# Kernel optimization log

Measured on AMD Instinct MI355X. Metric: run time of the kernel, lower is better.

## Reference

```python
import jax, jax.numpy as jnp
import numpy as np
from jax import lax

TAU = 0.1
EPS = 1e-10


def setup_inputs() -> dict:
    key = jax.random.key(0)
    ks = jax.random.split(key, 9)
    T, B, I, H, O = 512, 128, 512, 512, 512
    std = 1.0 / np.sqrt(H)
    x = jax.random.normal(ks[0], (T, B, I), dtype=jnp.float32)
    # uniform noise for per-step gumbel-softmax sampling (training mode)
    gumbel_u = jax.random.uniform(ks[1], (T, H, 2), dtype=jnp.float32,
                                  minval=1e-6, maxval=1.0 - 1e-6)
    # parameters (orthogonal init approximated by scaled normal)
    W_in = jax.random.normal(ks[2], (H, I), dtype=jnp.float32) * std
    b_in = jax.random.normal(ks[3], (H,), dtype=jnp.float32) * std
    Wrec_free = jax.nn.relu(jax.random.normal(ks[4], (H, H), dtype=jnp.float32) * std)
    rec_bias = jax.random.normal(ks[5], (H,), dtype=jnp.float32) * std
    eimask_logit = jax.random.normal(ks[6], (H, 2), dtype=jnp.float32)
    W_out = jax.random.normal(ks[7], (O, H), dtype=jnp.float32) * std
    b_out = jax.random.normal(ks[8], (O,), dtype=jnp.float32) * std
    return {"x": x, "gumbel_u": gumbel_u, "W_in": W_in, "b_in": b_in,
            "Wrec_free": Wrec_free, "rec_bias": rec_bias,
            "eimask_logit": eimask_logit, "W_out": W_out, "b_out": b_out}


def reference(x, gumbel_u, W_in, b_in, Wrec_free, rec_bias, eimask_logit, W_out, b_out):
    # x: (T, B, I); gumbel_u: (T, H, 2)
    B = x.shape[1]
    H = W_in.shape[0]
    # gumbel-softmax (soft, tau=0.1) per timestep -> ei code in [-1, 1]
    g = -jnp.log(-jnp.log(gumbel_u + EPS) + EPS)                 # (T, H, 2)
    mask = jax.nn.softmax((eimask_logit[None] + g) / TAU, axis=-1)
    ei = mask[..., 0] - mask[..., 1]                              # (T, H)
    Wrec = jax.nn.relu(Wrec_free)                                 # (H, H)
    # precompute input gate for all steps: (T, B, H)
    ig = jnp.einsum('tbi,hi->tbh', x, W_in) + b_in

    def step(h, inp):
        ig_t, ei_t = inp
        # h @ (Wrec @ diag(ei)).T == (h * ei) @ Wrec.T
        rec_in = (h * ei_t) @ Wrec.T + rec_bias
        h_new = jax.nn.softplus(ig_t + rec_in)
        return h_new, h_new

    h0 = jnp.zeros((B, H), dtype=x.dtype)
    h_last, hs = lax.scan(step, h0, (ig, ei))                     # hs: (T, B, H)
    outputs = jnp.einsum('tbh,oh->tbo', hs, W_out) + b_out        # (T, B, O)
    c_last = jnp.zeros_like(h_last)                               # c is never updated
    return outputs, h_last, c_last
```

## Files before the change

### kernel.cpp

```cpp
#include <hip/hip_runtime.h>
#include <stdint.h>


typedef __attribute__((ext_vector_type(8))) short short8;
typedef __attribute__((ext_vector_type(4))) float f32x4;
typedef __attribute__((ext_vector_type(4))) int int4x;

__device__ __forceinline__ unsigned short f2b(float f) {
  unsigned int u = __float_as_uint(f);
  u = (u + 0x7fffu + ((u >> 16) & 1u)) >> 16;
  return (unsigned short)u;
}
__device__ __forceinline__ float b2f(unsigned short s) {
  return __uint_as_float(((unsigned int)s) << 16);
}

__global__ void prep_kernel(const float* __restrict__ gu,
                            const float* __restrict__ logit,
                            const float* __restrict__ win,
                            const float* __restrict__ wout,
                            float* __restrict__ ei,
                            unsigned short* __restrict__ winb,
                            unsigned short* __restrict__ woutb,
                            float* __restrict__ c_last) {
  int i = blockIdx.x * 256 + threadIdx.x;
  int h = i & 511;
  float u0 = gu[2 * i], u1 = gu[2 * i + 1];
  float l0 = logit[2 * h], l1 = logit[2 * h + 1];
  float g0 = -logf(-logf(u0 + 1e-10f) + 1e-10f);
  float g1 = -logf(-logf(u1 + 1e-10f) + 1e-10f);
  float dz = ((l0 + g0) - (l1 + g1)) * 10.0f;
  ei[i] = tanhf(0.5f * dz);
  winb[i]  = f2b(win[i]);
  woutb[i] = f2b(wout[i]);
  if (i < 65536) c_last[i] = 0.0f;
}

__global__ void wquant_kernel(const float* __restrict__ wrec,
                              char* __restrict__ wrec8,
                              float* __restrict__ wscale) {
  const int n = blockIdx.x;
  const int l = threadIdx.x;
  const float* row = wrec + (size_t)n * 512 + l * 8;
  float v[8];
  float m = 0.f;
#pragma unroll
  for (int e = 0; e < 8; ++e) {
    v[e] = fmaxf(row[e], 0.f);
    m = fmaxf(m, v[e]);
  }
#pragma unroll
  for (int off = 32; off >= 1; off >>= 1) m = fmaxf(m, __shfl_down(m, off));
  m = __shfl(m, 0);
  const float s = (m > 0.f) ? (m / 127.f) : 1.f;
  const float inv = 1.f / s;
  unsigned long long pk = 0;
#pragma unroll
  for (int e = 0; e < 8; ++e) {
    int q = (int)rintf(v[e] * inv);
    pk |= ((unsigned long long)(unsigned char)(char)q) << (8 * e);
  }
  *(unsigned long long*)(wrec8 + (size_t)n * 512 + l * 8) = pk;
  if (l == 0) wscale[n] = s;
}

template <int A_F32, int OUT_BF16>
__global__ __launch_bounds__(256, 2) void gemm512(
    const void* __restrict__ Ap, const unsigned short* __restrict__ W,
    const float* __restrict__ bias, void* __restrict__ Cp) {
  __shared__ __align__(16) unsigned short Al[128][32];
  __shared__ __align__(16) unsigned short Bl[128][32];
  const int tid = threadIdx.x;
  const int w = tid >> 6, l = tid & 63;
  const int wr = w >> 1, wc = w & 1;
  const int lm = l & 15, lq = l >> 4;
  const size_t m0 = (size_t)blockIdx.x * 128;
  const int n0 = blockIdx.y * 128;
  const int r = tid >> 1;
  const int sb = (tid & 1) << 1;
  f32x4 acc[4][4] = {};

  for (int kt = 0; kt < 16; ++kt) {
    const int k0 = kt << 5;
    {
      char* dst = (char*)Al + r * 64;
      if (A_F32) {
        const float* A = (const float*)Ap + (m0 + r) * 512 + k0 + (sb << 3);
#pragma unroll
        for (int j = 0; j < 2; ++j) {
          float4 v0 = ((const float4*)A)[2 * j + 0];
          float4 v1 = ((const float4*)A)[2 * j + 1];
          short8 o;
          o[0] = (short)f2b(v0.x); o[1] = (short)f2b(v0.y);
          o[2] = (short)f2b(v0.z); o[3] = (short)f2b(v0.w);
          o[4] = (short)f2b(v1.x); o[5] = (short)f2b(v1.y);
          o[6] = (short)f2b(v1.z); o[7] = (short)f2b(v1.w);
          *(short8*)(dst + (((sb + j + (r >> 1)) & 3) << 4)) = o;
        }
      } else {
        const unsigned short* A =
            (const unsigned short*)Ap + (m0 + r) * 512 + k0 + (sb << 3);
#pragma unroll
        for (int j = 0; j < 2; ++j)
          *(short8*)(dst + (((sb + j + (r >> 1)) & 3) << 4)) =
              *(const short8*)(A + 8 * j);
      }
      const unsigned short* Wp = W + ((size_t)(n0 + r) << 9) + k0 + (sb << 3);
      char* dstB = (char*)Bl + r * 64;
#pragma unroll
      for (int j = 0; j < 2; ++j)
        *(short8*)(dstB + (((sb + j + (r >> 1)) & 3) << 4)) =
            *(const short8*)(Wp + 8 * j);
    }
    __syncthreads();
    short8 af[4], bf[4];
#pragma unroll
    for (int i = 0; i < 4; ++i) {
      int row = wr * 64 + i * 16 + lm;
      af[i] = *(const short8*)((char*)Al + row * 64 +
                               (((lq + (row >> 1)) & 3) << 4));
    }
#pragma unroll
    for (int j = 0; j < 4; ++j) {
      int row = wc * 64 + j * 16 + lm;
      bf[j] = *(const short8*)((char*)Bl + row * 64 +
                               (((lq + (row >> 1)) & 3) << 4));
    }
#pragma unroll
    for (int i = 0; i < 4; ++i)
#pragma unroll
      for (int j = 0; j < 4; ++j)
        acc[i][j] =
            __builtin_amdgcn_mfma_f32_16x16x32_bf16(af[i], bf[j], acc[i][j], 0, 0, 0);
    __syncthreads();
  }
  float bv[4];
#pragma unroll
  for (int j = 0; j < 4; ++j) bv[j] = bias[n0 + wc * 64 + j * 16 + lm];
#pragma unroll
  for (int i = 0; i < 4; ++i) {
#pragma unroll
    for (int r4 = 0; r4 < 4; ++r4) {
      size_t gm = m0 + wr * 64 + i * 16 + lq * 4 + r4;
#pragma unroll
      for (int j = 0; j < 4; ++j) {
        int gn = n0 + wc * 64 + j * 16 + lm;
        float v = acc[i][j][r4] + bv[j];
        if (OUT_BF16)
          ((unsigned short*)Cp)[(gm << 9) + gn] = f2b(v);
        else
          ((float*)Cp)[(gm << 9) + gn] = v;
      }
    }
  }
}

__global__ __launch_bounds__(512, 1) void recur9_kernel(
    const unsigned short* __restrict__ ig,
    const float* __restrict__ ei,
    const char* __restrict__ wrec8,
    const float* __restrict__ wscale,
    const float* __restrict__ rbias,
    unsigned short* __restrict__ hs,
    float* __restrict__ h_last) {
  __shared__ __align__(16) char As[2][16][512];
  __shared__ float Rls[8][68];
  const int tid = threadIdx.x;
  const int g = blockIdx.x;
  const int w = tid >> 6, l = tid & 63;
  const int lm = l & 15, lq = l >> 4;
  const int nbase = w << 6;
  const int lswz = lm & 7;
  const int n_own = nbase + l;

  int4x bregs[8][4];
#pragma unroll
  for (int kk = 0; kk < 8; ++kk)
#pragma unroll
    for (int j = 0; j < 4; ++j)
      bregs[kk][j] = *(const int4x*)(
          wrec8 + ((size_t)(nbase + j * 16 + lm) << 9) + (kk << 6) + (lq << 4));
  const float wscv = wscale[n_own] * 0.0625f;
  const float rbv  = rbias[n_own];
  {
    int4x z = {0, 0, 0, 0};
    *(int4x*)((char*)As + tid * 32) = z;
    *(int4x*)((char*)As + tid * 32 + 16) = z;
  }
  __syncthreads();

  const unsigned short* igp = ig + ((size_t)g << 9) + n_own;
  unsigned short ig_cur = igp[0];
  float ei_cur = ei[512 + n_own];

#pragma unroll 1
  for (int t = 0; t < 512; ++t) {
    const int par = t & 1, par2 = par ^ 1;
    unsigned short ig_nxt = 0;
    float ei_nxt = 0.f;
    if (t < 511)
      ig_nxt = __builtin_nontemporal_load(igp + (size_t)(t + 1) * 65536);
    if (t < 510) ei_nxt = ei[(size_t)(t + 2) * 512 + n_own];

    int4x acc[4] = {};
    const char* aRow = (const char*)As + par * 8192 + lm * 512;
#pragma unroll
    for (int kk = 0; kk < 8; ++kk) {
      int4x av = *(const int4x*)(aRow + ((((kk << 2) | lq) ^ lswz) << 4));
#pragma unroll
      for (int j = 0; j < 4; ++j)
        acc[j] = __builtin_amdgcn_mfma_i32_16x16x64_i8(av, bregs[kk][j],
                                                       acc[j], 0, 0, 0);
    }
    if (lq == 0) {
#pragma unroll
      for (int j = 0; j < 4; ++j) Rls[w][j * 17 + lm] = (float)acc[j][0];
    }
    float rec = Rls[w][lq * 17 + lm] * wscv;
    float z = rec + b2f(ig_cur) + rbv;
    float az = fabsf(z);
    float h = fmaxf(z, 0.f) + __logf(1.f + __expf(-az));
    if (t < 511) {
      float a = h * ei_cur * 16.f;
      int ai = (int)rintf(fminf(fmaxf(a, -127.f), 127.f));
      ((char*)As)[par2 * 8192 + n_own] = (char)ai;
    }
    __builtin_nontemporal_store(
        f2b(h), hs + (((size_t)t * 128 + g) << 9) + n_own);
    if (t == 511) h_last[((size_t)g << 9) + n_own] = h;
    ig_cur = ig_nxt;
    ei_cur = ei_nxt;
    __syncthreads();
  }
}

extern "C" void kernel_launch(void* const* d_in, const int* in_sizes, int n_in,
                              void* d_out, int out_size, void* d_ws,
                              size_t ws_size, hipStream_t stream) {
  const float* x     = (const float*)d_in[0];
  const float* gu    = (const float*)d_in[1];
  const float* Win   = (const float*)d_in[2];
  const float* bin   = (const float*)d_in[3];
  const float* Wrec  = (const float*)d_in[4];
  const float* rbias = (const float*)d_in[5];
  const float* elog  = (const float*)d_in[6];
  const float* Wout  = (const float*)d_in[7];
  const float* bout  = (const float*)d_in[8];

  char* ws = (char*)d_ws;
  float* ei             = (float*)ws;
  unsigned short* winb  = (unsigned short*)(ws + 4194304);
  unsigned short* woutb = (unsigned short*)(ws + 4718592);
  char* wrec8           = (char*)(ws + 5242880);
  float* wscale         = (float*)(ws + 5505024);
  unsigned short* igb   = (unsigned short*)(ws + 6291456);
  unsigned short* hs    = (unsigned short*)(ws + 73400320);

  float* outp  = (float*)d_out;
  float* hlast = outp + 33554432;
  float* clast = outp + 33554432 + 65536;

  prep_kernel<<<1024, 256, 0, stream>>>(gu, elog, Win, Wout, ei, winb, woutb,
                                        clast);
  wquant_kernel<<<512, 64, 0, stream>>>(Wrec, wrec8, wscale);
  gemm512<1, 1><<<dim3(512, 4), 256, 0, stream>>>(x, winb, bin, igb);
  recur9_kernel<<<128, 512, 0, stream>>>(igb, ei, wrec8, wscale, rbias, hs,
                                         hlast);
  gemm512<0, 0><<<dim3(512, 4), 256, 0, stream>>>(hs, woutb, bout, outp);
}
```

Baseline: 575.0 us.

## Replace MFMA recurrence matvec with per-thread int8 dot4 over register-resident weights

```diff
diff --git a/kernel.cpp b/kernel.cpp
--- a/kernel.cpp
+++ b/kernel.cpp
@@ -5,6 +5,18 @@
 typedef __attribute__((ext_vector_type(8))) short short8;
 typedef __attribute__((ext_vector_type(4))) float f32x4;
 typedef __attribute__((ext_vector_type(4))) int int4x;
+
+#if __has_builtin(__builtin_amdgcn_sdot4)
+#define SDOT4(a, b, c) __builtin_amdgcn_sdot4((a), (b), (c), false)
+#else
+__device__ __forceinline__ int sdot4_asm(int a, int b, int c) {
+  int r;
+  asm volatile("v_dot4_i32_i8 %0, %1, %2, %3"
+               : "=v"(r) : "v"(a), "v"(b), "v"(c));
+  return r;
+}
+#define SDOT4(a, b, c) sdot4_asm((a), (b), (c))
+#endif
 
 __device__ __forceinline__ unsigned short f2b(float f) {
   unsigned int u = __float_as_uint(f);
@@ -155,7 +167,7 @@
   }
 }
 
-__global__ __launch_bounds__(512, 1) void recur9_kernel(
+__global__ __launch_bounds__(512, 2) void recur11_kernel(
     const unsigned short* __restrict__ ig,
     const float* __restrict__ ei,
     const char* __restrict__ wrec8,
@@ -163,35 +175,23 @@
     const float* __restrict__ rbias,
     unsigned short* __restrict__ hs,
     float* __restrict__ h_last) {
-  __shared__ __align__(16) char As[2][16][512];
-  __shared__ float Rls[8][68];
+  __shared__ __align__(16) char As[2][512];
   const int tid = threadIdx.x;
   const int g = blockIdx.x;
-  const int w = tid >> 6, l = tid & 63;
-  const int lm = l & 15, lq = l >> 4;
-  const int nbase = w << 6;
-  const int lswz = lm & 7;
-  const int n_own = nbase + l;
-
-  int4x bregs[8][4];
-#pragma unroll
-  for (int kk = 0; kk < 8; ++kk)
-#pragma unroll
-    for (int j = 0; j < 4; ++j)
-      bregs[kk][j] = *(const int4x*)(
-          wrec8 + ((size_t)(nbase + j * 16 + lm) << 9) + (kk << 6) + (lq << 4));
-  const float wscv = wscale[n_own] * 0.0625f;
-  const float rbv  = rbias[n_own];
-  {
-    int4x z = {0, 0, 0, 0};
-    *(int4x*)((char*)As + tid * 32) = z;
-    *(int4x*)((char*)As + tid * 32 + 16) = z;
-  }
+  const int n = tid;
+
+  int4x wregs[32];
+#pragma unroll
+  for (int d = 0; d < 32; ++d)
+    wregs[d] = *(const int4x*)(wrec8 + ((size_t)n << 9) + (d << 4));
+  const float wscv = wscale[n] * 0.0625f;
+  const float rbv  = rbias[n];
+  if (tid < 256) ((int*)As)[tid] = 0;
   __syncthreads();
 
-  const unsigned short* igp = ig + ((size_t)g << 9) + n_own;
+  const unsigned short* igp = ig + ((size_t)g << 9) + n;
   unsigned short ig_cur = igp[0];
-  float ei_cur = ei[512 + n_own];
+  float ei_cur = ei[512 + n];
 
 #pragma unroll 1
   for (int t = 0; t < 512; ++t) {
@@ -200,34 +200,31 @@
     float ei_nxt = 0.f;
     if (t < 511)
       ig_nxt = __builtin_nontemporal_load(igp + (size_t)(t + 1) * 65536);
-    if (t < 510) ei_nxt = ei[(size_t)(t + 2) * 512 + n_own];
-
-    int4x acc[4] = {};
-    const char* aRow = (const char*)As + par * 8192 + lm * 512;
-#pragma unroll
-    for (int kk = 0; kk < 8; ++kk) {
-      int4x av = *(const int4x*)(aRow + ((((kk << 2) | lq) ^ lswz) << 4));
-#pragma unroll
-      for (int j = 0; j < 4; ++j)
-        acc[j] = __builtin_amdgcn_mfma_i32_16x16x64_i8(av, bregs[kk][j],
-                                                       acc[j], 0, 0, 0);
-    }
-    if (lq == 0) {
-#pragma unroll
-      for (int j = 0; j < 4; ++j) Rls[w][j * 17 + lm] = (float)acc[j][0];
-    }
-    float rec = Rls[w][lq * 17 + lm] * wscv;
-    float z = rec + b2f(ig_cur) + rbv;
+    if (t < 510) ei_nxt = ei[(size_t)(t + 2) * 512 + n];
+
+    const char* ap = &As[par][0];
+    int ac0 = 0, ac1 = 0, ac2 = 0, ac3 = 0;
+#pragma unroll
+    for (int d = 0; d < 32; ++d) {
+      int4x a4 = *(const int4x*)(ap + (d << 4));
+      ac0 = SDOT4(a4[0], wregs[d][0], ac0);
+      ac1 = SDOT4(a4[1], wregs[d][1], ac1);
+      ac2 = SDOT4(a4[2], wregs[d][2], ac2);
+      ac3 = SDOT4(a4[3], wregs[d][3], ac3);
+    }
+    const int acci = (ac0 + ac1) + (ac2 + ac3);
+
+    float z = (float)acci * wscv + b2f(ig_cur) + rbv;
     float az = fabsf(z);
     float h = fmaxf(z, 0.f) + __logf(1.f + __expf(-az));
     if (t < 511) {
       float a = h * ei_cur * 16.f;
       int ai = (int)rintf(fminf(fmaxf(a, -127.f), 127.f));
-      ((char*)As)[par2 * 8192 + n_own] = (char)ai;
-    }
-    __builtin_nontemporal_store(
-        f2b(h), hs + (((size_t)t * 128 + g) << 9) + n_own);
-    if (t == 511) h_last[((size_t)g << 9) + n_own] = h;
+      As[par2][n] = (char)ai;
+    }
+    __builtin_nontemporal_store(f2b(h),
+                                hs + (((size_t)t * 128 + g) << 9) + n);
+    if (t == 511) h_last[((size_t)g << 9) + n] = h;
     ig_cur = ig_nxt;
     ei_cur = ei_nxt;
     __syncthreads();
@@ -264,7 +261,7 @@
                                         clast);
   wquant_kernel<<<512, 64, 0, stream>>>(Wrec, wrec8, wscale);
   gemm512<1, 1><<<dim3(512, 4), 256, 0, stream>>>(x, winb, bin, igb);
-  recur9_kernel<<<128, 512, 0, stream>>>(igb, ei, wrec8, wscale, rbias, hs,
-                                         hlast);
+  recur11_kernel<<<128, 512, 0, stream>>>(igb, ei, wrec8, wscale, rbias, hs,
+                                          hlast);
   gemm512<0, 0><<<dim3(512, 4), 256, 0, stream>>>(hs, woutb, bout, outp);
 }
```

After: 600.0 us. +4.4%, slower.
